# Kernel tuning notes

Measured on AMD Instinct MI355X. Metric: run time of the kernel, lower is better.

Reference implementation:

```python
import jax, jax.numpy as jnp
import numpy as np
from jax import lax

BN_EPS = 1e-5
# shifts generated by _generate_shifts(8): dy outer loop, dx inner, skipping (0,0);
# circular_shift rolls shifts=(dx, dy) over dims (2, 3) i.e. dx->H axis, dy->W axis
SHIFTS = [(-1, -1), (0, -1), (1, -1), (-1, 0), (1, 0), (-1, 1), (0, 1), (1, 1)]


def setup_inputs() -> dict:
    key = jax.random.key(0)
    k1, k2 = jax.random.split(key)
    x = jax.random.normal(k1, (32, 128, 56, 56), dtype=jnp.float32)
    # 8 paths, each a 3x3 conv [O, I, kh, kw]
    W = jax.random.normal(k2, (8, 128, 128, 3, 3), dtype=jnp.float32) * 0.05
    gamma = jnp.ones((128,), dtype=jnp.float32)
    beta = jnp.zeros((128,), dtype=jnp.float32)
    return {"x": x, "W": W, "gamma": gamma, "beta": beta}


def _conv3x3(x, w):
    return lax.conv_general_dilated(
        x, w, window_strides=(1, 1), padding=((1, 1), (1, 1)),
        dimension_numbers=("NCHW", "OIHW", "NCHW"))


def reference(x, W, gamma, beta):
    # sum of 8 shifted-input 3x3 convs (accumulated, no stack materialized)
    out = _conv3x3(jnp.roll(x, SHIFTS[0], axis=(2, 3)), W[0])
    for i in range(1, len(SHIFTS)):
        out = out + _conv3x3(jnp.roll(x, SHIFTS[i], axis=(2, 3)), W[i])
    # BatchNorm2d, training-mode batch stats (biased variance), eps=1e-5
    mean = jnp.mean(out, axis=(0, 2, 3), keepdims=True)
    var = jnp.mean(jnp.square(out - mean), axis=(0, 2, 3), keepdims=True)
    out = (out - mean) * lax.rsqrt(var + BN_EPS)
    out = out * gamma.reshape(1, -1, 1, 1) + beta.reshape(1, -1, 1, 1)
    return out
```

## Files before the change

kernel.cpp:

```cpp
#include <hip/hip_runtime.h>
#include <hip/hip_bf16.h>


typedef __attribute__((ext_vector_type(8)))  short s16x8;
typedef __attribute__((ext_vector_type(16))) float f32x16;

__device__ __forceinline__ void gload16(const void* g, void* l) {
    __builtin_amdgcn_global_load_lds(
        (const __attribute__((address_space(1))) unsigned int*)g,
        (__attribute__((address_space(3))) unsigned int*)l, 16, 0, 0);
}

__device__ __forceinline__ unsigned short f2bf(float f) {
    __hip_bfloat16 h = __float2bfloat16(f);
    return *(unsigned short*)&h;
}

__global__ __launch_bounds__(256) void transpose_kernel(
    const float* __restrict__ x, unsigned short* __restrict__ xb,
    float* __restrict__ xcols) {
    __shared__ float xt[128][57];
    const int h = blockIdx.x, n = blockIdx.y, t = threadIdx.x;
    for (int it = 0; it < 28; ++it) {
        int idx = it * 256 + t;
        int c = idx / 56, w = idx % 56;
        xt[c][w] = x[(((size_t)n * 128 + c) * 56 + h) * 56 + w];
    }
    __syncthreads();
    for (int it = 0; it < 4; ++it) {
        int unit = it * 256 + t;
        if (unit < 896) {
            int w = unit >> 4, cu = unit & 15;
            unsigned short pk[8];
#pragma unroll
            for (int j = 0; j < 8; ++j) pk[j] = f2bf(xt[cu * 8 + j][w]);
            *(uint4*)(xb + ((((size_t)n * 56 + h) * 56 + w) * 128 + cu * 8)) = *(uint4*)pk;
        }
    }
    for (int it = 0; it < 2; ++it) {
        int idx = it * 256 + t;
        int c = idx & 127, w4 = idx >> 7;
        const int wmap[4] = {54, 55, 0, 1};
        xcols[(((size_t)n * 4 + w4) * 56 + h) * 128 + c] = xt[c][wmap[w4]];
    }
}

__global__ __launch_bounds__(256) void wprep_kernel(
    const float* __restrict__ W, unsigned short* __restrict__ Ap,
    float* __restrict__ U, float* __restrict__ Uc) {
    const int bx = blockIdx.x, t = threadIdx.x;
    const int dxs[8] = {-1, 0, 1, -1, 1, -1, 0, 1};
    const int dys[8] = {-1, -1, -1, 0, 0, 1, 1, 1};
    if (bx < 1600) {
        int idx = bx * 256 + t;
        int tap = idx % 25, oc = idx / 25, c = oc % 128, o = oc / 128;
        int a = tap / 5, b = tap % 5;
        float s = 0.f;
#pragma unroll
        for (int i = 0; i < 8; ++i) {
            int kh = a - 1 + dxs[i];
            int kw = b - 1 + dys[i];
            if (kh >= 0 && kh < 3 && kw >= 0 && kw < 3)
                s += W[(((size_t)i * 128 + o) * 128 + c) * 9 + kh * 3 + kw];
        }
        int chunk = c >> 4, k = c & 15, ku = k >> 3, j = k & 7, mo = o >> 5;
        size_t off = ((((size_t)chunk * 25 + tap) * 4 + mo) * 64 + (ku * 32 + (o & 31))) * 8 + j;
        Ap[off] = f2bf(s);
    } else if (bx < 1856) {
        int idx = (bx - 1600) * 256 + t;
        int c = idx % 128, o = (idx / 128) % 128, e = idx / 16384;
        float u[15];
#pragma unroll
        for (int k = 0; k < 15; ++k) u[k] = 0.f;
#pragma unroll
        for (int i = 0; i < 8; ++i) {
            if (e < 2) {
                int kh = (e == 0) ? 0 : 2;
                int hh = (e == 0) ? -1 : 56;
                int sr = (hh - dxs[i] + 56) % 56;
                int r = (e == 0) ? (sr == 54 ? 0 : sr == 55 ? 1 : 2)
                                 : (sr == 55 ? 0 : sr == 0 ? 1 : 2);
#pragma unroll
                for (int kw = 0; kw < 3; ++kw) {
                    int be = kw - 1 - dys[i] + 2;
                    u[r * 5 + be] += W[(((size_t)i * 128 + o) * 128 + c) * 9 + kh * 3 + kw];
                }
            } else {
                int kw = (e == 2) ? 0 : 2;
                int ww = (e == 2) ? -1 : 56;
                int sc = (ww - dys[i] + 56) % 56;
                int r = (e == 2) ? (sc == 54 ? 0 : sc == 55 ? 1 : 2)
                                 : (sc == 55 ? 0 : sc == 0 ? 1 : 2);
#pragma unroll
                for (int kh = 0; kh < 3; ++kh) {
                    int al = kh - 1 - dxs[i] + 2;
                    u[r * 5 + al] += W[(((size_t)i * 128 + o) * 128 + c) * 9 + kh * 3 + kw];
                }
            }
        }
#pragma unroll
        for (int k = 0; k < 15; ++k)
            U[(((size_t)e * 15 + k) * 128 + c) * 128 + o] = u[k];
    } else {
        int idx = (bx - 1856) * 256 + t;
        int c = idx % 128, o = (idx / 128) % 128, cr = idx / 16384;
        int hC = (cr >> 1) ? 55 : 0, wC = (cr & 1) ? 55 : 0;
        int khb = hC ? 2 : 0, kwb = wC ? 2 : 0;
        float v[9];
#pragma unroll
        for (int p = 0; p < 9; ++p) v[p] = 0.f;
#pragma unroll
        for (int i = 0; i < 8; ++i)
            v[(dxs[i] + 1) * 3 + (dys[i] + 1)] = W[(((size_t)i * 128 + o) * 128 + c) * 9 + khb * 3 + kwb];
#pragma unroll
        for (int p = 0; p < 9; ++p)
            Uc[(((size_t)cr * 9 + p) * 128 + c) * 128 + o] = v[p];
    }
}

__global__ __launch_bounds__(512, 1) void conv_mfma(
    const unsigned short* __restrict__ xb, const unsigned short* __restrict__ Ap,
    float* __restrict__ out, float* __restrict__ P) {
    __shared__ __align__(16) unsigned short lds[32768];
    const int tile = blockIdx.x, n = blockIdx.y;
    const int p0 = tile * 512;
    const int t = threadIdx.x, wv = t >> 6, lane = t & 63;
    const int og = wv >> 2, pg = wv & 3;
    const int hstart = p0 / 56 - 2;

    int vB[4];
    bool fval[4];
#pragma unroll
    for (int nn = 0; nn < 4; ++nn) {
        int px = p0 + pg * 128 + nn * 32 + (lane & 31);
        fval[nn] = px < 3136;
        if (px > 3135) px = 3135;
        int h = px / 56, w = px % 56;
        vB[nn] = (lane >> 5) * 16384 + ((h - hstart - 2) * 60 + w) * 16;
    }
    f32x16 acc[2][4];
#pragma unroll
    for (int mm = 0; mm < 2; ++mm)
#pragma unroll
        for (int nn = 0; nn < 4; ++nn)
#pragma unroll
            for (int r = 0; r < 16; ++r) acc[mm][nn][r] = 0.f;

    const unsigned short* xbn = xb + (size_t)n * 401408;
    const unsigned short* apw = Ap + (size_t)(og * 2) * 512 + lane * 8;

    auto stage_xs = [&](int ch, int buf) {
#pragma unroll
        for (int it = 0; it < 4; ++it) {
            int unit = it * 512 + t;
            int u = unit >> 10, ph = unit & 1023;
            if (ph > 899) ph = 899;
            int r = ph / 60, wc2 = ph % 60;
            int gh = hstart + r;
            gh += (gh < 0) ? 56 : 0;
            gh -= (gh >= 56) ? 56 : 0;
            int gw = wc2 - 2;
            gw += (gw < 0) ? 56 : 0;
            gw -= (gw >= 56) ? 56 : 0;
            gload16(xbn + (gh * 56 + gw) * 128 + ch * 16 + u * 8,
                    (char*)lds + buf * 32768 + (size_t)(it * 512 + wv * 64) * 16);
        }
    };

    stage_xs(0, 0);
    __syncthreads();

#pragma unroll 1
    for (int ch = 0; ch < 8; ++ch) {
        if (ch < 7) stage_xs(ch + 1, (ch + 1) & 1);
        const char* xsBase = (const char*)lds + (ch & 1) * 32768;
        const unsigned short* apc = apw + (size_t)ch * 51200;
#pragma unroll
        for (int tap = 0; tap < 25; ++tap) {
            const int toff = ((tap / 5) * 60 + (tap % 5)) * 16;
            s16x8 a0 = *(const s16x8*)(apc + (size_t)tap * 2048);
            s16x8 a1 = *(const s16x8*)(apc + (size_t)tap * 2048 + 512);
            s16x8 b0 = *(const s16x8*)(xsBase + vB[0] + toff);
            s16x8 b1 = *(const s16x8*)(xsBase + vB[1] + toff);
            s16x8 b2 = *(const s16x8*)(xsBase + vB[2] + toff);
            s16x8 b3 = *(const s16x8*)(xsBase + vB[3] + toff);
            acc[0][0] = __builtin_amdgcn_mfma_f32_32x32x16_bf16(a0, b0, acc[0][0], 0, 0, 0);
            acc[1][0] = __builtin_amdgcn_mfma_f32_32x32x16_bf16(a1, b0, acc[1][0], 0, 0, 0);
            acc[0][1] = __builtin_amdgcn_mfma_f32_32x32x16_bf16(a0, b1, acc[0][1], 0, 0, 0);
            acc[1][1] = __builtin_amdgcn_mfma_f32_32x32x16_bf16(a1, b1, acc[1][1], 0, 0, 0);
            acc[0][2] = __builtin_amdgcn_mfma_f32_32x32x16_bf16(a0, b2, acc[0][2], 0, 0, 0);
            acc[1][2] = __builtin_amdgcn_mfma_f32_32x32x16_bf16(a1, b2, acc[1][2], 0, 0, 0);
            acc[0][3] = __builtin_amdgcn_mfma_f32_32x32x16_bf16(a0, b3, acc[0][3], 0, 0, 0);
            acc[1][3] = __builtin_amdgcn_mfma_f32_32x32x16_bf16(a1, b3, acc[1][3], 0, 0, 0);
        }
        __syncthreads();
    }

    const int slot = (n * 7 + tile) * 4 + pg;
#pragma unroll
    for (int mm = 0; mm < 2; ++mm) {
#pragma unroll
        for (int r = 0; r < 16; ++r) {
            int o = og * 64 + mm * 32 + (r & 3) + ((lane >> 5) << 2) + ((r >> 2) << 3);
            float s = 0.f, q = 0.f;
#pragma unroll
            for (int nn = 0; nn < 4; ++nn) {
                if (fval[nn]) {
                    float v = acc[mm][nn][r];
                    size_t oi = ((size_t)(n * 128 + o)) * 3136 + (p0 + pg * 128 + nn * 32 + (lane & 31));
                    out[oi] = v;
                    s += v;
                    q = fmaf(v, v, q);
                }
            }
#pragma unroll
            for (int off = 1; off < 32; off <<= 1) {
                s += __shfl_xor(s, off);
                q += __shfl_xor(q, off);
            }
            if ((lane & 31) == 0) {
                P[((size_t)slot * 2 + 0) * 128 + o] = s;
                P[((size_t)slot * 2 + 1) * 128 + o] = q;
            }
        }
    }
}

__global__ __launch_bounds__(512) void border_kernel(
    const float* __restrict__ x, const float* __restrict__ xcols,
    const float* __restrict__ U,
    float* __restrict__ corrRow, float* __restrict__ corrCol) {
    __shared__ float xsb[3][128][33];
    __shared__ float red[2][2][64][15];
    const int e = blockIdx.x, n = blockIdx.y, part = blockIdx.z;
    const int t = threadIdx.x, lane = t & 63, wv = t >> 6;
    const int oh = wv & 1, qh = (wv >> 1) & 1, chalf = wv >> 2;
    int rows[3];
    if (e == 0 || e == 2) { rows[0] = 54; rows[1] = 55; rows[2] = 0; }
    else                  { rows[0] = 55; rows[1] = 0;  rows[2] = 1; }
    if (e < 2) {
        for (int it = 0; it < 24; ++it) {
            int idx = it * 512 + t;
            int m = idx & 31, c = (idx >> 5) & 127, r = idx >> 12;
            int g = part * 28 + m - 2;
            g += (g < 0) ? 56 : 0;
            g -= (g >= 56) ? 56 : 0;
            xsb[r][c][m] = x[(((size_t)n * 128 + c) * 56 + rows[r]) * 56 + g];
        }
    } else {
        int w4[3];
#pragma unroll
        for (int r = 0; r < 3; ++r)
            w4[r] = (rows[r] == 54) ? 0 : (rows[r] == 55) ? 1 : (rows[r] == 0) ? 2 : 3;
        for (int it = 0; it < 24; ++it) {
            int idx = it * 512 + t;
            int c = idx & 127, m = (idx >> 7) & 31, r = idx >> 12;
            int g = part * 28 + m - 2;
            g += (g < 0) ? 56 : 0;
            g -= (g >= 56) ? 56 : 0;
            xsb[r][c][m] = xcols[(((size_t)n * 4 + w4[r]) * 56 + g) * 128 + c];
        }
    }
    __syncthreads();
    const int o = oh * 64 + lane;
    const int pxl = qh * 14;
    float corr[14];
#pragma unroll
    for (int k = 0; k < 14; ++k) corr[k] = 0.f;
#pragma unroll 2
    for (int ci = 0; ci < 64; ++ci) {
        const int c = chalf * 64 + ci;
#pragma unroll
        for (int r = 0; r < 3; ++r) {
            float xl[18];
#pragma unroll
            for (int j = 0; j < 18; ++j) xl[j] = xsb[r][c][pxl + j];
#pragma unroll
            for (int be = 0; be < 5; ++be) {
                float u = U[(((size_t)e * 15 + r * 5 + be) * 128 + c) * 128 + o];
#pragma unroll
                for (int k = 0; k < 14; ++k) corr[k] = fmaf(u, xl[k + be], corr[k]);
            }
        }
    }
    if (chalf == 1) {
#pragma unroll
        for (int k = 0; k < 14; ++k) red[qh][oh][lane][k] = corr[k];
    }
    __syncthreads();
    if (chalf == 0) {
#pragma unroll
        for (int k = 0; k < 14; ++k) corr[k] += red[qh][oh][lane][k];
        const int pbase = part * 28 + qh * 14;
        float* dst = (e < 2 ? corrRow + (((size_t)e * 32 + n) * 128 + o) * 56
                            : corrCol + (((size_t)(e - 2) * 32 + n) * 128 + o) * 56) + pbase;
#pragma unroll
        for (int k = 0; k < 14; ++k) dst[k] = corr[k];
    }
}

__global__ __launch_bounds__(256) void corner_kernel(
    const float* __restrict__ xcols, const float* __restrict__ Uc,
    float* __restrict__ cadd) {
    __shared__ float xc[9][128];
    __shared__ float red[2][128];
    const int cr = blockIdx.x, n = blockIdx.y, t = threadIdx.x;
    const int hC = (cr >> 1) ? 55 : 0, wC = (cr & 1) ? 55 : 0;
    const int khb = hC ? 2 : 0, kwb = wC ? 2 : 0;
    for (int it = 0; it < 5; ++it) {
        int idx = it * 256 + t;
        if (idx < 1152) {
            int c = idx & 127, p = idx >> 7;
            int di = p / 3, dj = p % 3;
            int hs = (hC + khb - 1 - (di - 1) + 56) % 56;
            int ws = (wC + kwb - 1 - (dj - 1) + 56) % 56;
            int w4 = (ws == 54) ? 0 : (ws == 55) ? 1 : (ws == 0) ? 2 : 3;
            xc[p][c] = xcols[(((size_t)n * 4 + w4) * 56 + hs) * 128 + c];
        }
    }
    __syncthreads();
    const int o = t & 127, half = t >> 7;
    float corr = 0.f;
    const float* ucb = Uc + ((size_t)cr * 9 * 128) * 128 + o;
#pragma unroll 4
    for (int pc = half * 576; pc < half * 576 + 576; ++pc) {
        int p = pc >> 7, c = pc & 127;
        corr = fmaf(ucb[(size_t)pc * 128], xc[p][c], corr);
    }
    red[half][o] = corr;
    __syncthreads();
    if (t < 128)
        cadd[(size_t)cr * 4096 + n * 128 + t] = red[0][t] + red[1][t];
}

__global__ __launch_bounds__(256) void finalize_kernel(
    const float* __restrict__ P, const float* __restrict__ out,
    const float* __restrict__ corrRow, const float* __restrict__ corrCol,
    const float* __restrict__ cadd,
    const float* __restrict__ gamma, const float* __restrict__ beta,
    float* __restrict__ SS) {
    const int c = blockIdx.x, t = threadIdx.x;
    float s = 0.f, q = 0.f;
    for (int sl = t; sl < 896; sl += 256) {
        s += P[((size_t)sl * 2 + 0) * 128 + c];
        q += P[((size_t)sl * 2 + 1) * 128 + c];
    }
    for (int item = t; item < 7040; item += 256) {
        int n = item / 220, bidx = item % 220;
        int h, w;
        if (bidx < 56)       { h = 0;  w = bidx; }
        else if (bidx < 112) { h = 55; w = bidx - 56; }
        else if (bidx < 166) { w = 0;  h = bidx - 111; }
        else                 { w = 55; h = bidx - 165; }
        float d = 0.f;
        if (h == 0)  d -= corrRow[(((size_t)0 * 32 + n) * 128 + c) * 56 + w];
        if (h == 55) d -= corrRow[(((size_t)1 * 32 + n) * 128 + c) * 56 + w];
        if (w == 0)  d -= corrCol[(((size_t)0 * 32 + n) * 128 + c) * 56 + h];
        if (w == 55) d -= corrCol[(((size_t)1 * 32 + n) * 128 + c) * 56 + h];
        if ((h == 0 || h == 55) && (w == 0 || w == 55)) {
            int cr = (h ? 2 : 0) + (w ? 1 : 0);
            d += cadd[(size_t)cr * 4096 + n * 128 + c];
        }
        float old = out[((size_t)(n * 128 + c)) * 3136 + h * 56 + w];
        s += d;
        q += d * d + 2.f * old * d;
    }
    __shared__ float rs[256], rq[256];
    rs[t] = s; rq[t] = q;
    __syncthreads();
    for (int st = 128; st > 0; st >>= 1) {
        if (t < st) { rs[t] += rs[t + st]; rq[t] += rq[t + st]; }
        __syncthreads();
    }
    if (t == 0) {
        const float inv = 1.f / 100352.f;
        float mean = rs[0] * inv;
        float var  = rq[0] * inv - mean * mean;
        float sc = gamma[c] * rsqrtf(var + 1e-5f);
        SS[c] = sc;
        SS[128 + c] = beta[c] - mean * sc;
    }
}

__global__ __launch_bounds__(256) void bn_apply_kernel(
    float* __restrict__ out, const float* __restrict__ SS,
    const float* __restrict__ corrRow, const float* __restrict__ corrCol,
    const float* __restrict__ cadd) {
    size_t idx = (size_t)blockIdx.x * 256 + threadIdx.x;
    int plane = (int)(idx / 784);
    int rem = (int)(idx % 784);
    int h = rem / 14, w4 = (rem % 14) * 4;
    int c = plane & 127, n = plane >> 7;
    float sc = SS[c], sh = SS[128 + c];
    float4 v = ((float4*)out)[idx];
    float d0 = 0.f, d1 = 0.f, d2 = 0.f, d3 = 0.f;
    if (h == 0 || h == 55) {
        int eh = (h == 55) ? 1 : 0;
        const float4 cr4 = *(const float4*)(corrRow + (((size_t)eh * 32 + n) * 128 + c) * 56 + w4);
        d0 -= cr4.x; d1 -= cr4.y; d2 -= cr4.z; d3 -= cr4.w;
    }
    if (w4 == 0)  d0 -= corrCol[(((size_t)0 * 32 + n) * 128 + c) * 56 + h];
    if (w4 == 52) d3 -= corrCol[(((size_t)1 * 32 + n) * 128 + c) * 56 + h];
    if (h == 0 || h == 55) {
        int hb = (h == 55) ? 2 : 0;
        if (w4 == 0)  d0 += cadd[(size_t)(hb + 0) * 4096 + n * 128 + c];
        if (w4 == 52) d3 += cadd[(size_t)(hb + 1) * 4096 + n * 128 + c];
    }
    v.x = fmaf(v.x + d0, sc, sh);
    v.y = fmaf(v.y + d1, sc, sh);
    v.z = fmaf(v.z + d2, sc, sh);
    v.w = fmaf(v.w + d3, sc, sh);
    ((float4*)out)[idx] = v;
}

extern "C" void kernel_launch(void* const* d_in, const int* in_sizes, int n_in,
                              void* d_out, int out_size, void* d_ws, size_t ws_size,
                              hipStream_t stream) {
    const float* x     = (const float*)d_in[0];
    const float* W     = (const float*)d_in[1];
    const float* gamma = (const float*)d_in[2];
    const float* beta  = (const float*)d_in[3];
    float* out = (float*)d_out;

    char* ws = (char*)d_ws;
    unsigned short* xb = (unsigned short*)ws;
    unsigned short* Ap = (unsigned short*)(ws + 25690112);
    float* U       = (float*)(ws + 26513408);
    float* Uc      = (float*)(ws + 30445568);
    float* P       = (float*)(ws + 32804864);
    float* SS      = (float*)(ws + 34017280);
    float* xcols   = (float*)(ws + 34018304);
    float* corrRow = (float*)(ws + 37688320);
    float* corrCol = (float*)(ws + 39523328);
    float* cadd    = (float*)(ws + 41358336);

    transpose_kernel<<<dim3(56, 32), 256, 0, stream>>>(x, xb, xcols);
    wprep_kernel<<<2112, 256, 0, stream>>>(W, Ap, U, Uc);
    conv_mfma<<<dim3(7, 32), 512, 0, stream>>>(xb, Ap, out, P);
    border_kernel<<<dim3(4, 32, 2), 512, 0, stream>>>(x, xcols, U, corrRow, corrCol);
    corner_kernel<<<dim3(4, 32), 256, 0, stream>>>(xcols, Uc, cadd);
    finalize_kernel<<<128, 256, 0, stream>>>(P, out, corrRow, corrCol, cadd, gamma, beta, SS);
    bn_apply_kernel<<<12544, 256, 0, stream>>>(out, SS, corrRow, corrCol, cadd);
}
```

Baseline: 315.9 us.

## Merge prep kernels and fuse conv, border and corner work into one launch

```diff
diff --git a/kernel.cpp b/kernel.cpp
--- a/kernel.cpp
+++ b/kernel.cpp
@@ -16,43 +16,43 @@
     return *(unsigned short*)&h;
 }
 
-__global__ __launch_bounds__(256) void transpose_kernel(
-    const float* __restrict__ x, unsigned short* __restrict__ xb,
-    float* __restrict__ xcols) {
+__global__ __launch_bounds__(256) void prep_kernel(
+    const float* __restrict__ x, const float* __restrict__ W,
+    unsigned short* __restrict__ xb, float* __restrict__ xcols,
+    unsigned short* __restrict__ Ap, float* __restrict__ U, float* __restrict__ Uc) {
     __shared__ float xt[128][57];
-    const int h = blockIdx.x, n = blockIdx.y, t = threadIdx.x;
-    for (int it = 0; it < 28; ++it) {
-        int idx = it * 256 + t;
-        int c = idx / 56, w = idx % 56;
-        xt[c][w] = x[(((size_t)n * 128 + c) * 56 + h) * 56 + w];
-    }
-    __syncthreads();
-    for (int it = 0; it < 4; ++it) {
-        int unit = it * 256 + t;
-        if (unit < 896) {
-            int w = unit >> 4, cu = unit & 15;
-            unsigned short pk[8];
-#pragma unroll
-            for (int j = 0; j < 8; ++j) pk[j] = f2bf(xt[cu * 8 + j][w]);
-            *(uint4*)(xb + ((((size_t)n * 56 + h) * 56 + w) * 128 + cu * 8)) = *(uint4*)pk;
-        }
-    }
-    for (int it = 0; it < 2; ++it) {
-        int idx = it * 256 + t;
-        int c = idx & 127, w4 = idx >> 7;
-        const int wmap[4] = {54, 55, 0, 1};
-        xcols[(((size_t)n * 4 + w4) * 56 + h) * 128 + c] = xt[c][wmap[w4]];
-    }
-}
-
-__global__ __launch_bounds__(256) void wprep_kernel(
-    const float* __restrict__ W, unsigned short* __restrict__ Ap,
-    float* __restrict__ U, float* __restrict__ Uc) {
     const int bx = blockIdx.x, t = threadIdx.x;
     const int dxs[8] = {-1, 0, 1, -1, 1, -1, 0, 1};
     const int dys[8] = {-1, -1, -1, 0, 0, 1, 1, 1};
-    if (bx < 1600) {
-        int idx = bx * 256 + t;
+    if (bx < 1792) {
+        const int h = bx % 56, n = bx / 56;
+        for (int it = 0; it < 28; ++it) {
+            int idx = it * 256 + t;
+            int c = idx / 56, w = idx % 56;
+            xt[c][w] = x[(((size_t)n * 128 + c) * 56 + h) * 56 + w];
+        }
+        __syncthreads();
+        for (int it = 0; it < 4; ++it) {
+            int unit = it * 256 + t;
+            if (unit < 896) {
+                int w = unit >> 4, cu = unit & 15;
+                unsigned short pk[8];
+#pragma unroll
+                for (int j = 0; j < 8; ++j) pk[j] = f2bf(xt[cu * 8 + j][w]);
+                *(uint4*)(xb + ((((size_t)n * 56 + h) * 56 + w) * 128 + cu * 8)) = *(uint4*)pk;
+            }
+        }
+        for (int it = 0; it < 2; ++it) {
+            int idx = it * 256 + t;
+            int c = idx & 127, w4 = idx >> 7;
+            const int wmap[4] = {54, 55, 0, 1};
+            xcols[(((size_t)n * 4 + w4) * 56 + h) * 128 + c] = xt[c][wmap[w4]];
+        }
+        return;
+    }
+    const int bxw = bx - 1792;
+    if (bxw < 1600) {
+        int idx = bxw * 256 + t;
         int tap = idx % 25, oc = idx / 25, c = oc % 128, o = oc / 128;
         int a = tap / 5, b = tap % 5;
         float s = 0.f;
@@ -66,8 +66,8 @@
         int chunk = c >> 4, k = c & 15, ku = k >> 3, j = k & 7, mo = o >> 5;
         size_t off = ((((size_t)chunk * 25 + tap) * 4 + mo) * 64 + (ku * 32 + (o & 31))) * 8 + j;
         Ap[off] = f2bf(s);
-    } else if (bx < 1856) {
-        int idx = (bx - 1600) * 256 + t;
+    } else if (bxw < 1856) {
+        int idx = (bxw - 1600) * 256 + t;
         int c = idx % 128, o = (idx / 128) % 128, e = idx / 16384;
         float u[15];
 #pragma unroll
@@ -102,7 +102,7 @@
         for (int k = 0; k < 15; ++k)
             U[(((size_t)e * 15 + k) * 128 + c) * 128 + o] = u[k];
     } else {
-        int idx = (bx - 1856) * 256 + t;
+        int idx = (bxw - 1856) * 256 + t;
         int c = idx % 128, o = (idx / 128) % 128, cr = idx / 16384;
         int hC = (cr >> 1) ? 55 : 0, wC = (cr & 1) ? 55 : 0;
         int khb = hC ? 2 : 0, kwb = wC ? 2 : 0;
@@ -118,219 +118,221 @@
     }
 }
 
-__global__ __launch_bounds__(512, 1) void conv_mfma(
+__global__ __launch_bounds__(512, 4) void main_kernel(
     const unsigned short* __restrict__ xb, const unsigned short* __restrict__ Ap,
-    float* __restrict__ out, float* __restrict__ P) {
-    __shared__ __align__(16) unsigned short lds[32768];
-    const int tile = blockIdx.x, n = blockIdx.y;
-    const int p0 = tile * 512;
+    const float* __restrict__ x, const float* __restrict__ xcols,
+    const float* __restrict__ U, const float* __restrict__ Uc,
+    float* __restrict__ out, float* __restrict__ P,
+    float* __restrict__ corrRow, float* __restrict__ corrCol,
+    float* __restrict__ cadd) {
+    __shared__ __align__(16) char smem[66048];
+    const int bx = blockIdx.x, n = blockIdx.y;
     const int t = threadIdx.x, wv = t >> 6, lane = t & 63;
-    const int og = wv >> 2, pg = wv & 3;
-    const int hstart = p0 / 56 - 2;
-
-    int vB[4];
-    bool fval[4];
-#pragma unroll
-    for (int nn = 0; nn < 4; ++nn) {
-        int px = p0 + pg * 128 + nn * 32 + (lane & 31);
-        fval[nn] = px < 3136;
-        if (px > 3135) px = 3135;
-        int h = px / 56, w = px % 56;
-        vB[nn] = (lane >> 5) * 16384 + ((h - hstart - 2) * 60 + w) * 16;
-    }
-    f32x16 acc[2][4];
-#pragma unroll
-    for (int mm = 0; mm < 2; ++mm)
-#pragma unroll
-        for (int nn = 0; nn < 4; ++nn)
-#pragma unroll
-            for (int r = 0; r < 16; ++r) acc[mm][nn][r] = 0.f;
-
-    const unsigned short* xbn = xb + (size_t)n * 401408;
-    const unsigned short* apw = Ap + (size_t)(og * 2) * 512 + lane * 8;
-
-    auto stage_xs = [&](int ch, int buf) {
-#pragma unroll
-        for (int it = 0; it < 4; ++it) {
-            int unit = it * 512 + t;
-            int u = unit >> 10, ph = unit & 1023;
-            if (ph > 899) ph = 899;
-            int r = ph / 60, wc2 = ph % 60;
-            int gh = hstart + r;
-            gh += (gh < 0) ? 56 : 0;
-            gh -= (gh >= 56) ? 56 : 0;
-            int gw = wc2 - 2;
-            gw += (gw < 0) ? 56 : 0;
-            gw -= (gw >= 56) ? 56 : 0;
-            gload16(xbn + (gh * 56 + gw) * 128 + ch * 16 + u * 8,
-                    (char*)lds + buf * 32768 + (size_t)(it * 512 + wv * 64) * 16);
-        }
-    };
-
-    stage_xs(0, 0);
-    __syncthreads();
+
+    if (bx < 13) {
+        const int tile = bx;
+        const int p0 = tile * 256;
+        const int hstart = p0 / 56 - 2;
+        const int og = wv >> 2, pg = wv & 3;
+        int vB[2];
+        bool fval[2];
+#pragma unroll
+        for (int nn = 0; nn < 2; ++nn) {
+            int px = p0 + pg * 64 + nn * 32 + (lane & 31);
+            fval[nn] = px < 3136;
+            if (px > 3135) px = 3135;
+            int h = px / 56, w = px % 56;
+            vB[nn] = (lane >> 5) * 10240 + ((h - hstart - 2) * 60 + w) * 16;
+        }
+        f32x16 acc[2][2];
+#pragma unroll
+        for (int mm = 0; mm < 2; ++mm)
+#pragma unroll
+            for (int nn = 0; nn < 2; ++nn)
+#pragma unroll
+                for (int r = 0; r < 16; ++r) acc[mm][nn][r] = 0.f;
+
+        const unsigned short* xbn = xb + (size_t)n * 401408;
+        const unsigned short* apw = Ap + (size_t)(og * 2) * 512 + lane * 8;
+
+        auto stage_xs = [&](int ch, int buf) {
+#pragma unroll
+            for (int it = 0; it < 3; ++it) {
+                int base = it * 512 + wv * 64;
+                if (base < 1280) {
+                    int unit = base + lane;
+                    int u = (unit >= 640) ? 1 : 0;
+                    int ph = unit - u * 640;
+                    if (ph > 599) ph = 599;
+                    int r = ph / 60, wc2 = ph % 60;
+                    int gh = hstart + r;
+                    gh += (gh < 0) ? 56 : 0;
+                    gh -= (gh >= 56) ? 56 : 0;
+                    int gw = wc2 - 2;
+                    gw += (gw < 0) ? 56 : 0;
+                    gw -= (gw >= 56) ? 56 : 0;
+                    gload16(xbn + (gh * 56 + gw) * 128 + ch * 16 + u * 8,
+                            smem + buf * 20480 + (size_t)base * 16);
+                }
+            }
+        };
+
+        stage_xs(0, 0);
+        __syncthreads();
 
 #pragma unroll 1
-    for (int ch = 0; ch < 8; ++ch) {
-        if (ch < 7) stage_xs(ch + 1, (ch + 1) & 1);
-        const char* xsBase = (const char*)lds + (ch & 1) * 32768;
-        const unsigned short* apc = apw + (size_t)ch * 51200;
-#pragma unroll
-        for (int tap = 0; tap < 25; ++tap) {
-            const int toff = ((tap / 5) * 60 + (tap % 5)) * 16;
-            s16x8 a0 = *(const s16x8*)(apc + (size_t)tap * 2048);
-            s16x8 a1 = *(const s16x8*)(apc + (size_t)tap * 2048 + 512);
-            s16x8 b0 = *(const s16x8*)(xsBase + vB[0] + toff);
-            s16x8 b1 = *(const s16x8*)(xsBase + vB[1] + toff);
-            s16x8 b2 = *(const s16x8*)(xsBase + vB[2] + toff);
-            s16x8 b3 = *(const s16x8*)(xsBase + vB[3] + toff);
-            acc[0][0] = __builtin_amdgcn_mfma_f32_32x32x16_bf16(a0, b0, acc[0][0], 0, 0, 0);
-            acc[1][0] = __builtin_amdgcn_mfma_f32_32x32x16_bf16(a1, b0, acc[1][0], 0, 0, 0);
-            acc[0][1] = __builtin_amdgcn_mfma_f32_32x32x16_bf16(a0, b1, acc[0][1], 0, 0, 0);
-            acc[1][1] = __builtin_amdgcn_mfma_f32_32x32x16_bf16(a1, b1, acc[1][1], 0, 0, 0);
-            acc[0][2] = __builtin_amdgcn_mfma_f32_32x32x16_bf16(a0, b2, acc[0][2], 0, 0, 0);
-            acc[1][2] = __builtin_amdgcn_mfma_f32_32x32x16_bf16(a1, b2, acc[1][2], 0, 0, 0);
-            acc[0][3] = __builtin_amdgcn_mfma_f32_32x32x16_bf16(a0, b3, acc[0][3], 0, 0, 0);
-            acc[1][3] = __builtin_amdgcn_mfma_f32_32x32x16_bf16(a1, b3, acc[1][3], 0, 0, 0);
-        }
-        __syncthreads();
-    }
-
-    const int slot = (n * 7 + tile) * 4 + pg;
-#pragma unroll
-    for (int mm = 0; mm < 2; ++mm) {
-#pragma unroll
-        for (int r = 0; r < 16; ++r) {
-            int o = og * 64 + mm * 32 + (r & 3) + ((lane >> 5) << 2) + ((r >> 2) << 3);
-            float s = 0.f, q = 0.f;
-#pragma unroll
-            for (int nn = 0; nn < 4; ++nn) {
-                if (fval[nn]) {
-                    float v = acc[mm][nn][r];
-                    size_t oi = ((size_t)(n * 128 + o)) * 3136 + (p0 + pg * 128 + nn * 32 + (lane & 31));
-                    out[oi] = v;
-                    s += v;
-                    q = fmaf(v, v, q);
-                }
-            }
-#pragma unroll
-            for (int off = 1; off < 32; off <<= 1) {
-                s += __shfl_xor(s, off);
-                q += __shfl_xor(q, off);
-            }
-            if ((lane & 31) == 0) {
-                P[((size_t)slot * 2 + 0) * 128 + o] = s;
-                P[((size_t)slot * 2 + 1) * 128 + o] = q;
-            }
-        }
-    }
-}
-
-__global__ __launch_bounds__(512) void border_kernel(
-    const float* __restrict__ x, const float* __restrict__ xcols,
-    const float* __restrict__ U,
-    float* __restrict__ corrRow, float* __restrict__ corrCol) {
-    __shared__ float xsb[3][128][33];
-    __shared__ float red[2][2][64][15];
-    const int e = blockIdx.x, n = blockIdx.y, part = blockIdx.z;
-    const int t = threadIdx.x, lane = t & 63, wv = t >> 6;
-    const int oh = wv & 1, qh = (wv >> 1) & 1, chalf = wv >> 2;
-    int rows[3];
-    if (e == 0 || e == 2) { rows[0] = 54; rows[1] = 55; rows[2] = 0; }
-    else                  { rows[0] = 55; rows[1] = 0;  rows[2] = 1; }
-    if (e < 2) {
-        for (int it = 0; it < 24; ++it) {
+        for (int ch = 0; ch < 8; ++ch) {
+            if (ch < 7) stage_xs(ch + 1, (ch + 1) & 1);
+            const char* xsBase = (const char*)smem + (ch & 1) * 20480;
+            const unsigned short* apc = apw + (size_t)ch * 51200;
+#pragma unroll
+            for (int tap = 0; tap < 25; ++tap) {
+                const int toff = ((tap / 5) * 60 + (tap % 5)) * 16;
+                s16x8 a0 = *(const s16x8*)(apc + (size_t)tap * 2048);
+                s16x8 a1 = *(const s16x8*)(apc + (size_t)tap * 2048 + 512);
+                s16x8 b0 = *(const s16x8*)(xsBase + vB[0] + toff);
+                s16x8 b1 = *(const s16x8*)(xsBase + vB[1] + toff);
+                acc[0][0] = __builtin_amdgcn_mfma_f32_32x32x16_bf16(a0, b0, acc[0][0], 0, 0, 0);
+                acc[1][0] = __builtin_amdgcn_mfma_f32_32x32x16_bf16(a1, b0, acc[1][0], 0, 0, 0);
+                acc[0][1] = __builtin_amdgcn_mfma_f32_32x32x16_bf16(a0, b1, acc[0][1], 0, 0, 0);
+                acc[1][1] = __builtin_amdgcn_mfma_f32_32x32x16_bf16(a1, b1, acc[1][1], 0, 0, 0);
+            }
+            __syncthreads();
+        }
+
+        float* redc = (float*)smem;
+        const int slot = n * 13 + tile;
+#pragma unroll
+        for (int mm = 0; mm < 2; ++mm) {
+#pragma unroll
+            for (int r = 0; r < 16; ++r) {
+                int o = og * 64 + mm * 32 + (r & 3) + ((lane >> 5) << 2) + ((r >> 2) << 3);
+                float s = 0.f, q = 0.f;
+#pragma unroll
+                for (int nn = 0; nn < 2; ++nn) {
+                    if (fval[nn]) {
+                        float v = acc[mm][nn][r];
+                        size_t oi = ((size_t)(n * 128 + o)) * 3136 + (p0 + pg * 64 + nn * 32 + (lane & 31));
+                        out[oi] = v;
+                        s += v;
+                        q = fmaf(v, v, q);
+                    }
+                }
+#pragma unroll
+                for (int off = 1; off < 32; off <<= 1) {
+                    s += __shfl_xor(s, off);
+                    q += __shfl_xor(q, off);
+                }
+                if ((lane & 31) == 0) {
+                    redc[pg * 128 + o] = s;
+                    redc[512 + pg * 128 + o] = q;
+                }
+            }
+        }
+        __syncthreads();
+        if (t < 256) {
+            int o = t & 127, which = t >> 7;
+            const float* rb = redc + which * 512;
+            P[((size_t)slot * 2 + which) * 128 + o] = rb[o] + rb[128 + o] + rb[256 + o] + rb[384 + o];
+        }
+        return;
+    }
+
+    if (bx < 21) {
+        float (*xsb)[128][33] = reinterpret_cast<float(*)[128][33]>(smem);
+        float (*red)[2][64][15] = reinterpret_cast<float(*)[2][64][15]>(smem + 50688);
+        const int idx0 = bx - 13;
+        const int e = idx0 >> 1, part = idx0 & 1;
+        const int oh = wv & 1, qh = (wv >> 1) & 1, chalf = wv >> 2;
+        int rows[3];
+        if (e == 0 || e == 2) { rows[0] = 54; rows[1] = 55; rows[2] = 0; }
+        else                  { rows[0] = 55; rows[1] = 0;  rows[2] = 1; }
+        if (e < 2) {
+            for (int it = 0; it < 24; ++it) {
+                int idx = it * 512 + t;
+                int m = idx & 31, c = (idx >> 5) & 127, r = idx >> 12;
+                int g = part * 28 + m - 2;
+                g += (g < 0) ? 56 : 0;
+                g -= (g >= 56) ? 56 : 0;
+                xsb[r][c][m] = x[(((size_t)n * 128 + c) * 56 + rows[r]) * 56 + g];
+            }
+        } else {
+            int w4[3];
+#pragma unroll
+            for (int r = 0; r < 3; ++r)
+                w4[r] = (rows[r] == 54) ? 0 : (rows[r] == 55) ? 1 : (rows[r] == 0) ? 2 : 3;
+            for (int it = 0; it < 24; ++it) {
+                int idx = it * 512 + t;
+                int c = idx & 127, m = (idx >> 7) & 31, r = idx >> 12;
+                int g = part * 28 + m - 2;
+                g += (g < 0) ? 56 : 0;
+                g -= (g >= 56) ? 56 : 0;
+                xsb[r][c][m] = xcols[(((size_t)n * 4 + w4[r]) * 56 + g) * 128 + c];
+            }
+        }
+        __syncthreads();
+        const int o = oh * 64 + lane;
+        const int pxl = qh * 14;
+        float corr[14];
+#pragma unroll
+        for (int k = 0; k < 14; ++k) corr[k] = 0.f;
+#pragma unroll 2
+        for (int ci = 0; ci < 64; ++ci) {
+            const int c = chalf * 64 + ci;
+#pragma unroll
+            for (int r = 0; r < 3; ++r) {
+                float xl[18];
+#pragma unroll
+                for (int j = 0; j < 18; ++j) xl[j] = xsb[r][c][pxl + j];
+#pragma unroll
+                for (int be = 0; be < 5; ++be) {
+                    float u = U[(((size_t)e * 15 + r * 5 + be) * 128 + c) * 128 + o];
+#pragma unroll
+                    for (int k = 0; k < 14; ++k) corr[k] = fmaf(u, xl[k + be], corr[k]);
+                }
+            }
+        }
+        if (chalf == 1) {
+#pragma unroll
+            for (int k = 0; k < 14; ++k) red[qh][oh][lane][k] = corr[k];
+        }
+        __syncthreads();
+        if (chalf == 0) {
+#pragma unroll
+            for (int k = 0; k < 14; ++k) corr[k] += red[qh][oh][lane][k];
+            const int pbase = part * 28 + qh * 14;
+            float* dst = (e < 2 ? corrRow + (((size_t)e * 32 + n) * 128 + o) * 56
+                                : corrCol + (((size_t)(e - 2) * 32 + n) * 128 + o) * 56) + pbase;
+#pragma unroll
+            for (int k = 0; k < 14; ++k) dst[k] = corr[k];
+        }
+        return;
+    }
+
+    {
+        float (*xc)[128] = reinterpret_cast<float(*)[128]>(smem);
+        for (int it = 0; it < 9; ++it) {
             int idx = it * 512 + t;
-            int m = idx & 31, c = (idx >> 5) & 127, r = idx >> 12;
-            int g = part * 28 + m - 2;
-            g += (g < 0) ? 56 : 0;
-            g -= (g >= 56) ? 56 : 0;
-            xsb[r][c][m] = x[(((size_t)n * 128 + c) * 56 + rows[r]) * 56 + g];
-        }
-    } else {
-        int w4[3];
-#pragma unroll
-        for (int r = 0; r < 3; ++r)
-            w4[r] = (rows[r] == 54) ? 0 : (rows[r] == 55) ? 1 : (rows[r] == 0) ? 2 : 3;
-        for (int it = 0; it < 24; ++it) {
-            int idx = it * 512 + t;
-            int c = idx & 127, m = (idx >> 7) & 31, r = idx >> 12;
-            int g = part * 28 + m - 2;
-            g += (g < 0) ? 56 : 0;
-            g -= (g >= 56) ? 56 : 0;
-            xsb[r][c][m] = xcols[(((size_t)n * 4 + w4[r]) * 56 + g) * 128 + c];
-        }
-    }
-    __syncthreads();
-    const int o = oh * 64 + lane;
-    const int pxl = qh * 14;
-    float corr[14];
-#pragma unroll
-    for (int k = 0; k < 14; ++k) corr[k] = 0.f;
-#pragma unroll 2
-    for (int ci = 0; ci < 64; ++ci) {
-        const int c = chalf * 64 + ci;
-#pragma unroll
-        for (int r = 0; r < 3; ++r) {
-            float xl[18];
-#pragma unroll
-            for (int j = 0; j < 18; ++j) xl[j] = xsb[r][c][pxl + j];
-#pragma unroll
-            for (int be = 0; be < 5; ++be) {
-                float u = U[(((size_t)e * 15 + r * 5 + be) * 128 + c) * 128 + o];
-#pragma unroll
-                for (int k = 0; k < 14; ++k) corr[k] = fmaf(u, xl[k + be], corr[k]);
-            }
-        }
-    }
-    if (chalf == 1) {
-#pragma unroll
-        for (int k = 0; k < 14; ++k) red[qh][oh][lane][k] = corr[k];
-    }
-    __syncthreads();
-    if (chalf == 0) {
-#pragma unroll
-        for (int k = 0; k < 14; ++k) corr[k] += red[qh][oh][lane][k];
-        const int pbase = part * 28 + qh * 14;
-        float* dst = (e < 2 ? corrRow + (((size_t)e * 32 + n) * 128 + o) * 56
-                            : corrCol + (((size_t)(e - 2) * 32 + n) * 128 + o) * 56) + pbase;
-#pragma unroll
-        for (int k = 0; k < 14; ++k) dst[k] = corr[k];
-    }
-}
-
-__global__ __launch_bounds__(256) void corner_kernel(
-    const float* __restrict__ xcols, const float* __restrict__ Uc,
-    float* __restrict__ cadd) {
-    __shared__ float xc[9][128];
-    __shared__ float red[2][128];
-    const int cr = blockIdx.x, n = blockIdx.y, t = threadIdx.x;
-    const int hC = (cr >> 1) ? 55 : 0, wC = (cr & 1) ? 55 : 0;
-    const int khb = hC ? 2 : 0, kwb = wC ? 2 : 0;
-    for (int it = 0; it < 5; ++it) {
-        int idx = it * 256 + t;
-        if (idx < 1152) {
-            int c = idx & 127, p = idx >> 7;
+            int c = idx & 127, p = (idx >> 7) % 9, cr = idx / 1152;
             int di = p / 3, dj = p % 3;
+            int hC = (cr >> 1) ? 55 : 0, wC = (cr & 1) ? 55 : 0;
+            int khb = hC ? 2 : 0, kwb = wC ? 2 : 0;
             int hs = (hC + khb - 1 - (di - 1) + 56) % 56;
             int ws = (wC + kwb - 1 - (dj - 1) + 56) % 56;
             int w4 = (ws == 54) ? 0 : (ws == 55) ? 1 : (ws == 0) ? 2 : 3;
-            xc[p][c] = xcols[(((size_t)n * 4 + w4) * 56 + hs) * 128 + c];
-        }
-    }
-    __syncthreads();
-    const int o = t & 127, half = t >> 7;
-    float corr = 0.f;
-    const float* ucb = Uc + ((size_t)cr * 9 * 128) * 128 + o;
+            xc[cr * 9 + p][c] = xcols[(((size_t)n * 4 + w4) * 56 + hs) * 128 + c];
+        }
+        __syncthreads();
+        const int cr = t >> 7, o = t & 127;
+        float corr = 0.f;
+        const float* ucb = Uc + ((size_t)cr * 9 * 128) * 128 + o;
 #pragma unroll 4
-    for (int pc = half * 576; pc < half * 576 + 576; ++pc) {
-        int p = pc >> 7, c = pc & 127;
-        corr = fmaf(ucb[(size_t)pc * 128], xc[p][c], corr);
-    }
-    red[half][o] = corr;
-    __syncthreads();
-    if (t < 128)
-        cadd[(size_t)cr * 4096 + n * 128 + t] = red[0][t] + red[1][t];
+        for (int pc = 0; pc < 1152; ++pc) {
+            int p = pc >> 7, c = pc & 127;
+            corr = fmaf(ucb[(size_t)pc * 128], xc[cr * 9 + p][c], corr);
+        }
+        cadd[(size_t)cr * 4096 + n * 128 + o] = corr;
+    }
 }
 
 __global__ __launch_bounds__(256) void finalize_kernel(
@@ -341,7 +343,7 @@
     float* __restrict__ SS) {
     const int c = blockIdx.x, t = threadIdx.x;
     float s = 0.f, q = 0.f;
-    for (int sl = t; sl < 896; sl += 256) {
+    for (int sl = t; sl < 416; sl += 256) {
         s += P[((size_t)sl * 2 + 0) * 128 + c];
         q += P[((size_t)sl * 2 + 1) * 128 + c];
     }
@@ -434,11 +436,9 @@
     float* corrCol = (float*)(ws + 39523328);
     float* cadd    = (float*)(ws + 41358336);
 
-    transpose_kernel<<<dim3(56, 32), 256, 0, stream>>>(x, xb, xcols);
-    wprep_kernel<<<2112, 256, 0, stream>>>(W, Ap, U, Uc);
-    conv_mfma<<<dim3(7, 32), 512, 0, stream>>>(xb, Ap, out, P);
-    border_kernel<<<dim3(4, 32, 2), 512, 0, stream>>>(x, xcols, U, corrRow, corrCol);
-    corner_kernel<<<dim3(4, 32), 256, 0, stream>>>(xcols, Uc, cadd);
+    prep_kernel<<<3904, 256, 0, stream>>>(x, W, xb, xcols, Ap, U, Uc);
+    main_kernel<<<dim3(22, 32), 512, 0, stream>>>(xb, Ap, x, xcols, U, Uc,
+                                                  out, P, corrRow, corrCol, cadd);
     finalize_kernel<<<128, 256, 0, stream>>>(P, out, corrRow, corrCol, cadd, gamma, beta, SS);
     bn_apply_kernel<<<12544, 256, 0, stream>>>(out, SS, corrRow, corrCol, cadd);
 }
```

Result: faster. 281.5 us (-10.9%).
